# Optimization experiments

Measured on AMD Instinct MI355X. Metric: run time of the kernel, lower is better.

## Reference

```python
import jax, jax.numpy as jnp
import numpy as np

SIGMA = 25.0
HID, EMB = 64, 32
NBOX, BS = 10, 512
NPG = 3 * NBOX          # nodes per graph
N = BS * NPG            # total nodes


def _mlp2(h, W1, b1, W2, b2):
    return jax.nn.relu(h @ W1 + b1) @ W2 + b2


def _edge_conv(x, src, dst, W1, b1, W2, b2, n_nodes):
    # PyG EdgeConv: message = nn(cat([x_i, x_j - x_i])), aggr='max' at target i=dst
    xi = x[dst]
    xj = x[src]
    msg = _mlp2(jnp.concatenate([xi, xj - xi], axis=-1), W1, b1, W2, b2)
    return jax.ops.segment_max(msg, dst, num_segments=n_nodes)


def setup_inputs() -> dict:
    key = jax.random.key(0)
    k = jax.random.split(key, 16)
    w = lambda i, shape, s=0.1: jax.random.normal(k[i], shape, jnp.float32) * s
    # fully-connected directed edges (no self loops) within each of BS graphs
    ii, jj = np.meshgrid(np.arange(NPG), np.arange(NPG), indexing='ij')
    m = ii != jj
    off = (np.arange(BS) * NPG)[:, None]
    src = (ii[m][None, :] + off).reshape(-1)
    dst = (jj[m][None, :] + off).reshape(-1)
    edge_index = jnp.asarray(np.stack([src, dst]), dtype=jnp.int32)
    return {
        "x": jax.random.normal(k[0], (N, 2), jnp.float32),
        "t": jax.random.uniform(k[1], (BS, 1), jnp.float32, 1e-3, 1.0),
        "edge_index": edge_index,
        "n_box": NBOX,
        "gfp_W": jax.random.normal(k[2], (EMB // 2,), jnp.float32) * 30.0,
        "embed_W": w(3, (EMB, EMB)), "embed_b": jnp.zeros((EMB,), jnp.float32),
        "cat_emb": w(4, (3, EMB), 1.0), "cat_W": w(5, (EMB, EMB)), "cat_b": jnp.zeros((EMB,), jnp.float32),
        "init_W1": w(6, (2, HID)), "init_b1": jnp.zeros((HID,), jnp.float32),
        "init_W2": w(7, (HID, HID)), "init_b2": jnp.zeros((HID,), jnp.float32),
        "m1_W1": w(8, (2 * (HID + EMB), HID)), "m1_b1": jnp.zeros((HID,), jnp.float32),
        "m1_W2": w(9, (HID, HID)), "m1_b2": jnp.zeros((HID,), jnp.float32),
        "m2_W1": w(10, (2 * HID + 2 * EMB, HID)), "m2_b1": jnp.zeros((HID,), jnp.float32),
        "m2_W2": w(11, (HID, HID)), "m2_b2": jnp.zeros((HID,), jnp.float32),
        "m3_W1": w(12, (2 * HID + 2 * EMB, HID)), "m3_b1": jnp.zeros((HID,), jnp.float32),
        "m3_W2": w(13, (HID, 2)), "m3_b2": jnp.zeros((2,), jnp.float32),
    }


def reference(x, t, edge_index, n_box, gfp_W, embed_W, embed_b, cat_emb, cat_W, cat_b,
              init_W1, init_b1, init_W2, init_b2,
              m1_W1, m1_b1, m1_W2, m1_b2,
              m2_W1, m2_b1, m2_W2, m2_b2,
              m3_W1, m3_b1, m3_W2, m3_b2):
    n_nodes = x.shape[0]
    bs = t.shape[0]
    npg = 3 * n_box
    src, dst = edge_index[0], edge_index[1]
    # category embedding (mode='target'): pattern [0..0,1..1,2..2] tiled over graphs
    categories = jnp.tile(jnp.repeat(jnp.arange(3), n_box), bs)
    class_feat = jax.nn.relu(cat_emb[categories]) @ cat_W + cat_b          # [N, EMB]
    init_feat = jnp.concatenate(
        [_mlp2(x, init_W1, init_b1, init_W2, init_b2), class_feat], axis=-1)  # [N, HID+EMB]
    # Gaussian Fourier time embedding
    tp = t[:, 0]
    proj = tp[:, None] * gfp_W[None, :] * (2.0 * np.float32(np.pi))
    gfp = jnp.concatenate([jnp.sin(proj), jnp.cos(proj)], axis=-1)          # [bs, EMB]
    x_sigma = jax.nn.relu(jax.nn.relu(gfp) @ embed_W + embed_b)             # [bs, EMB]
    x_sigma = jnp.repeat(x_sigma, npg, axis=0)                              # [N, EMB]
    h = jax.nn.relu(_edge_conv(init_feat, src, dst, m1_W1, m1_b1, m1_W2, m1_b2, n_nodes))
    h = jnp.concatenate([h, x_sigma], axis=-1)
    h = jax.nn.relu(_edge_conv(h, src, dst, m2_W1, m2_b1, m2_W2, m2_b2, n_nodes))
    h = jnp.concatenate([h, x_sigma], axis=-1)
    h = _edge_conv(h, src, dst, m3_W1, m3_b1, m3_W2, m3_b2, n_nodes)        # [N, 2]
    # marginal_prob_std(t) = sqrt((sigma^{2t}-1)/(2 ln sigma)) per node
    t_node = jnp.repeat(tp, npg)[:, None]
    log_s = jnp.float32(np.log(SIGMA))
    std = jnp.sqrt((jnp.exp(2.0 * t_node * log_s) - 1.0) / (2.0 * log_s))
    return h / (std + 1e-7)
```

## Files before the change

kernel.cpp:

```cpp
#include <hip/hip_runtime.h>
#include <math.h>

constexpr int NPG  = 30;
constexpr int HID  = 64;
constexpr int EMB  = 32;
constexpr int FEAT = HID + EMB;
constexpr int BS   = 512;
constexpr int FROWH = 104;
constexpr int PROW  = 36;

constexpr int OFF_IW2  = 0;
constexpr int OFF_W1_1 = 4096;
constexpr int OFF_W1_2 = 16384;
constexpr int OFF_W1_3 = 28672;
constexpr int OFF_W2_1 = 40960;
constexpr int OFF_W2_2 = 45056;
constexpr int OFF_W2_3 = 49152;
constexpr int NHALF    = 51200;

typedef _Float16 half8 __attribute__((ext_vector_type(8)));
typedef __fp16   fp16x2 __attribute__((ext_vector_type(2)));
typedef float    f32x16 __attribute__((ext_vector_type(16)));

union HU  { unsigned u[4]; half8 h; };
union PK  { fp16x2 h2; unsigned u; };
union UPK { unsigned u; _Float16 h[2]; };

__device__ __forceinline__ void split8(const float* mv, half8& ah, half8& al) {
    #pragma unroll
    for (int d = 0; d < 4; d++) {
        auto ph = __builtin_amdgcn_cvt_pkrtz(mv[2*d], mv[2*d+1]);
        ah[2*d] = ph[0]; ah[2*d+1] = ph[1];
        float l0 = mv[2*d]   - (float)ph[0];
        float l1 = mv[2*d+1] - (float)ph[1];
        auto pl = __builtin_amdgcn_cvt_pkrtz(l0, l1);
        al[2*d] = pl[0]; al[2*d+1] = pl[1];
    }
}

__device__ __forceinline__ unsigned pkrne(float lo, float hi) {
    unsigned r;
    asm("v_fma_mixlo_f16 %0, %1, 1.0, 0" : "=v"(r) : "v"(lo));
    asm("v_fma_mixhi_f16 %0, %1, 1.0, 0" : "+v"(r) : "v"(hi));
    return r;
}

__device__ __forceinline__ unsigned pk_relu_add(unsigned a, unsigned b) {
    unsigned r;
    asm("v_pk_add_f16 %0, %1, %2" : "=v"(r) : "v"(a), "v"(b));
    asm("v_pk_max_f16 %0, %0, 0" : "+v"(r));
    return r;
}

__device__ __forceinline__ float dpp_xor1(float x) {
    return __int_as_float(__builtin_amdgcn_update_dpp(
        0, __float_as_int(x), 0xB1, 0xF, 0xF, true));
}

__global__ __launch_bounds__(256) void precompute_kernel(
    const float* __restrict__ t,
    const float* __restrict__ gfpW,
    const float* __restrict__ embW,
    const float* __restrict__ embb,
    const float* __restrict__ cat_emb,
    const float* __restrict__ catW,
    const float* __restrict__ catb,
    float* __restrict__ xs,
    float* __restrict__ cf3,
    float* __restrict__ stdv)
{
    int tid = blockIdx.x * blockDim.x + threadIdx.x;
    if (tid < BS) {
        float tp = t[tid];
        const float log_s = 3.2188758248682006f;
        stdv[tid] = sqrtf((expf(2.f * tp * log_s) - 1.f) / (2.f * log_s));

        float g[EMB];
        #pragma unroll
        for (int k = 0; k < EMB / 2; k++) {
            float pr = tp * gfpW[k] * 6.283185307179586f;
            g[k]           = sinf(pr);
            g[k + EMB / 2] = cosf(pr);
        }
        #pragma unroll
        for (int c = 0; c < EMB; c++) g[c] = fmaxf(g[c], 0.f);

        for (int o = 0; o < EMB; o++) {
            float acc = embb[o];
            #pragma unroll
            for (int c = 0; c < EMB; c++) acc = fmaf(g[c], embW[c * EMB + o], acc);
            xs[tid * EMB + o] = fmaxf(acc, 0.f);
        }
    } else if (tid < BS + 3 * EMB) {
        int idx = tid - BS;
        int r = idx >> 5, o = idx & 31;
        float acc = catb[o];
        #pragma unroll
        for (int c = 0; c < EMB; c++)
            acc = fmaf(fmaxf(cat_emb[r * EMB + c], 0.f), catW[c * EMB + o], acc);
        cf3[idx] = acc;
    }
}

__global__ __launch_bounds__(256) void convert_weights(
    const float* __restrict__ iW2,
    const float* __restrict__ W1_1, const float* __restrict__ W1_2,
    const float* __restrict__ W1_3,
    const float* __restrict__ W2_1, const float* __restrict__ W2_2,
    const float* __restrict__ W2_3,
    _Float16* __restrict__ outh)
{
    int idx = blockIdx.x * 256 + threadIdx.x;
    if (idx >= NHALF) return;
    float v;
    if (idx < OFF_W1_1) {
        int r = idx;
        int e = r & 7, cw = (r >> 3) & 31, hi = (r >> 8) & 1;
        int ks = (r >> 9) & 3, n = r >> 11;
        v = iW2[(16 * ks + 8 * hi + e) * HID + 32 * n + cw];
    } else if (idx < OFF_W2_1) {
        int r = idx - OFF_W1_1;
        int m = r / 12288; r %= 12288;
        const float* W1 = (m == 0) ? W1_1 : (m == 1) ? W1_2 : W1_3;
        int e = r & 7, cw = (r >> 3) & 31, hi = (r >> 8) & 1;
        int t2 = r >> 9;
        int ks = t2 % 6, np = t2 / 6;
        int rowoff = (np >= 2) ? FEAT : 0;
        int coloff = 32 * (np & 1);
        v = W1[(rowoff + 16 * ks + 8 * hi + e) * HID + coloff + cw];
    } else if (idx < OFF_W2_3) {
        int r = idx - OFF_W2_1;
        int m = r / 4096; r %= 4096;
        const float* W2 = (m == 0) ? W2_1 : W2_2;
        int e = r & 7, cw = (r >> 3) & 31, hi = (r >> 8) & 1;
        int ks = (r >> 9) & 3, n = r >> 11;
        v = W2[(16 * ks + 8 * hi + e) * HID + 32 * n + cw];
    } else {
        int r = idx - OFF_W2_3;
        int e = r & 7, cw = (r >> 3) & 31, hi = (r >> 8) & 1;
        int ks = (r >> 9) & 3;
        v = (cw < 2) ? W2_3[(16 * ks + 8 * hi + e) * 2 + cw] : 0.f;
    }
    outh[idx] = (_Float16)v;
}

__global__ __launch_bounds__(512, 4) void gnn_kernel(
    const float* __restrict__ xg,
    const float* __restrict__ iW1, const float* __restrict__ ib1,
    const float* __restrict__ ib2,
    const float* __restrict__ b1_1, const float* __restrict__ b2_1,
    const float* __restrict__ b1_2, const float* __restrict__ b2_2,
    const float* __restrict__ b1_3, const float* __restrict__ b2_3,
    const _Float16* __restrict__ hw,
    const float* __restrict__ xs_g,
    const float* __restrict__ cf3g,
    const float* __restrict__ stdv,
    float* __restrict__ out)
{
    const int g    = blockIdx.x;
    const int tid  = threadIdx.x;
    const int w    = tid >> 6;
    const int lane = tid & 63;
    const int cw   = lane & 31;
    const int hi   = lane >> 5;
    const int base = g * NPG;

    __shared__ __align__(16) unsigned slab[16 * 8 * 64];
    __shared__ __align__(16) _Float16 ftileh[32][FROWH];
    __shared__ __align__(16) unsigned ABp[32 * PROW];
    __shared__ __align__(16) unsigned Bp[32 * PROW];
    __shared__ float xs_s[EMB];

    float* slab32 = (float*)slab;

    if (tid < EMB) xs_s[tid] = xs_g[g * EMB + tid];

    if (w < 2) {
        int r = cw;
        float x0 = 0.f, x1 = 0.f;
        if (r < NPG) { x0 = xg[(base + r) * 2]; x1 = xg[(base + r) * 2 + 1]; }
        int n = w, coloff = 32 * n;
        f32x16 cc;
        #pragma unroll
        for (int z = 0; z < 16; z++) cc[z] = 0.f;
        #pragma unroll
        for (int ks = 0; ks < 4; ks++) {
            float mv[8];
            #pragma unroll
            for (int e = 0; e < 8; e++) {
                int k = 16 * ks + 8 * hi + e;
                mv[e] = fmaxf(fmaf(x1, iW1[HID + k], fmaf(x0, iW1[k], ib1[k])), 0.f);
            }
            half8 ah, al;
            split8(mv, ah, al);
            half8 wf = *(const half8*)&hw[OFF_IW2 + (((n * 4 + ks) * 2 + hi) * 32 + cw) * 8];
            cc = __builtin_amdgcn_mfma_f32_32x32x16_f16(ah, wf, cc, 0, 0, 0);
            cc = __builtin_amdgcn_mfma_f32_32x32x16_f16(al, wf, cc, 0, 0, 0);
        }
        float b2v = ib2[coloff + cw];
        #pragma unroll
        for (int rr = 0; rr < 16; rr++) {
            int row = (rr & 3) + 8 * (rr >> 2) + 4 * hi;
            if (row < NPG) ftileh[row][coloff + cw] = (_Float16)(cc[rr] + b2v);
        }
    }
    #pragma unroll
    for (int m = 0; m < 2; m++) {
        int idx = tid + 512 * m;
        if (idx < NPG * EMB) {
            int rr2 = idx >> 5, cc2 = idx & 31;
            ftileh[rr2][64 + cc2] = (_Float16)cf3g[(rr2 / 10) * EMB + cc2];
        }
    }
    __syncthreads();

    auto phase1AB = [&](const _Float16* __restrict__ W1f,
                        const float* __restrict__ b1) {
        if (w < 2) {
            const int n = __builtin_amdgcn_readfirstlane(w);
            f32x16 cA, cB;
            #pragma unroll
            for (int z = 0; z < 16; z++) { cA[z] = 0.f; cB[z] = 0.f; }
            #pragma unroll
            for (int ks = 0; ks < 6; ks++) {
                half8 af  = *(const half8*)&ftileh[cw][16 * ks + 8 * hi];
                half8 wfA = *(const half8*)&W1f[(((n * 6 + ks) * 2 + hi) * 32 + cw) * 8];
                half8 wfB = *(const half8*)&W1f[((((2 + n) * 6 + ks) * 2 + hi) * 32 + cw) * 8];
                cA = __builtin_amdgcn_mfma_f32_32x32x16_f16(af, wfA, cA, 0, 0, 0);
                cB = __builtin_amdgcn_mfma_f32_32x32x16_f16(af, wfB, cB, 0, 0, 0);
            }
            float b1v = b1[32 * n + cw];
            #pragma unroll
            for (int rr = 0; rr < 16; rr++) {
                float ab  = cA[rr] + b1v - cB[rr];
                float bb  = cB[rr];
                float abn = dpp_xor1(ab);
                float bbn = dpp_xor1(bb);
                int row = (rr & 3) + 8 * (rr >> 2) + 4 * hi;
                if ((cw & 1) == 0 && row < NPG) {
                    int idx = row * PROW + 16 * n + (cw >> 1);
                    ABp[idx] = pkrne(ab, abn);
                    Bp[idx]  = pkrne(bb, bbn);
                }
            }
        }
    };

    auto phase2_12 = [&](const half8 (&wf)[2][4], const float* __restrict__ b2) {
        const int s8 = __builtin_amdgcn_readfirstlane(w);
        float b2v[2] = { b2[cw], b2[32 + cw] };
        uint4 abp[4];
        #pragma unroll
        for (int ks = 0; ks < 4; ks++)
            abp[ks] = *(const uint4*)&ABp[cw * PROW + 8 * ks + 4 * hi];
        unsigned mxp[2][8];
        #pragma unroll
        for (int n = 0; n < 2; n++)
            #pragma unroll
            for (int d = 0; d < 8; d++) mxp[n][d] = 0xFC00FC00u;
        const bool selfh = (hi == ((s8 >> 2) & 1));

        #pragma unroll
        for (int m = 0; m < 4; m++) {
            int i = s8 + 8 * m;
            if (i < NPG) {
                const unsigned* bp = &Bp[i * PROW + 4 * hi];
                half8 am[4];
                #pragma unroll
                for (int ks = 0; ks < 4; ks++) {
                    uint4 bq = *(const uint4*)(bp + 8 * ks);
                    HU u;
                    u.u[0] = pk_relu_add(abp[ks].x, bq.x);
                    u.u[1] = pk_relu_add(abp[ks].y, bq.y);
                    u.u[2] = pk_relu_add(abp[ks].z, bq.z);
                    u.u[3] = pk_relu_add(abp[ks].w, bq.w);
                    am[ks] = u.h;
                }
                #pragma unroll
                for (int n = 0; n < 2; n++) {
                    f32x16 c;
                    #pragma unroll
                    for (int z = 0; z < 16; z++) c[z] = b2v[n];
                    #pragma unroll
                    for (int ks = 0; ks < 4; ks++)
                        c = __builtin_amdgcn_mfma_f32_32x32x16_f16(am[ks], wf[n][ks], c, 0, 0, 0);
                    switch (s8 & 3) {
                        case 0: c[4*m+0] = selfh ? -3.0e38f : c[4*m+0]; break;
                        case 1: c[4*m+1] = selfh ? -3.0e38f : c[4*m+1]; break;
                        case 2: c[4*m+2] = selfh ? -3.0e38f : c[4*m+2]; break;
                        default: c[4*m+3] = selfh ? -3.0e38f : c[4*m+3]; break;
                    }
                    #pragma unroll
                    for (int d = 0; d < 8; d++) {
                        PK pk; pk.h2 = __builtin_amdgcn_cvt_pkrtz(c[2*d], c[2*d+1]);
                        asm("v_pk_max_f16 %0, %0, %1" : "+v"(mxp[n][d]) : "v"(pk.u));
                    }
                }
            }
        }
        #pragma unroll
        for (int n = 0; n < 2; n++)
            #pragma unroll
            for (int d = 0; d < 8; d++)
                slab[(((n * 8 + d) * 8) + w) * 64 + lane] = mxp[n][d];
    };

    auto merge_12 = [&](bool installXS) {
        int rlane = tid & 63, rcw = rlane & 31, rhi = rlane >> 5;
        #pragma unroll
        for (int hh = 0; hh < 2; hh++) {
            int nd = (tid >> 6) + 8 * hh;
            unsigned mv = slab[(nd * 8 + 0) * 64 + rlane];
            #pragma unroll
            for (int ww = 1; ww < 8; ww++) {
                unsigned s = slab[(nd * 8 + ww) * 64 + rlane];
                asm("v_pk_max_f16 %0, %0, %1" : "+v"(mv) : "v"(s));
            }
            int n = nd >> 3, d = nd & 7;
            int col = 32 * n + rcw;
            UPK uu; uu.u = mv;
            int r0 = (2 * d & 3) + 8 * (d >> 1) + 4 * rhi;
            float v0 = fmaxf((float)uu.h[0], 0.f);
            float v1 = fmaxf((float)uu.h[1], 0.f);
            if (r0 < NPG)     ftileh[r0][col]     = (_Float16)v0;
            if (r0 + 1 < NPG) ftileh[r0 + 1][col] = (_Float16)v1;
        }
        if (installXS) {
            #pragma unroll
            for (int m = 0; m < 2; m++) {
                int idx = tid + 512 * m;
                if (idx < NPG * EMB) {
                    int rr2 = idx >> 5, cc2 = idx & 31;
                    ftileh[rr2][64 + cc2] = (_Float16)xs_s[cc2];
                }
            }
        }
    };

    {
        half8 wf[2][4];
        #pragma unroll
        for (int n = 0; n < 2; n++)
            #pragma unroll
            for (int ks = 0; ks < 4; ks++)
                wf[n][ks] = *(const half8*)&hw[OFF_W2_1 + (((n * 4 + ks) * 2 + hi) * 32 + cw) * 8];
        phase1AB(hw + OFF_W1_1, b1_1);
        __syncthreads();
        phase2_12(wf, b2_1);
        __syncthreads();
        merge_12(true);
        __syncthreads();
    }
    {
        half8 wf[2][4];
        #pragma unroll
        for (int n = 0; n < 2; n++)
            #pragma unroll
            for (int ks = 0; ks < 4; ks++)
                wf[n][ks] = *(const half8*)&hw[OFF_W2_2 + (((n * 4 + ks) * 2 + hi) * 32 + cw) * 8];
        phase1AB(hw + OFF_W1_2, b1_2);
        __syncthreads();
        phase2_12(wf, b2_2);
        __syncthreads();
        merge_12(false);
        __syncthreads();
    }
    {
        half8 wf3[4];
        #pragma unroll
        for (int ks = 0; ks < 4; ks++)
            wf3[ks] = *(const half8*)&hw[OFF_W2_3 + ((ks * 2 + hi) * 32 + cw) * 8];
        phase1AB(hw + OFF_W1_3, b1_3);
        __syncthreads();

        const int s8 = __builtin_amdgcn_readfirstlane(w);
        uint4 abp[4];
        #pragma unroll
        for (int ks = 0; ks < 4; ks++)
            abp[ks] = *(const uint4*)&ABp[cw * PROW + 8 * ks + 4 * hi];
        f32x16 mx;
        #pragma unroll
        for (int z = 0; z < 16; z++) mx[z] = -3.0e38f;
        const bool selfh = (hi == ((s8 >> 2) & 1));

        #pragma unroll
        for (int m = 0; m < 4; m++) {
            int i = s8 + 8 * m;
            if (i < NPG) {
                const unsigned* bp = &Bp[i * PROW + 4 * hi];
                f32x16 c;
                #pragma unroll
                for (int z = 0; z < 16; z++) c[z] = 0.f;
                #pragma unroll
                for (int ks = 0; ks < 4; ks++) {
                    uint4 bq = *(const uint4*)(bp + 8 * ks);
                    HU u;
                    u.u[0] = pk_relu_add(abp[ks].x, bq.x);
                    u.u[1] = pk_relu_add(abp[ks].y, bq.y);
                    u.u[2] = pk_relu_add(abp[ks].z, bq.z);
                    u.u[3] = pk_relu_add(abp[ks].w, bq.w);
                    c = __builtin_amdgcn_mfma_f32_32x32x16_f16(u.h, wf3[ks], c, 0, 0, 0);
                }
                switch (s8 & 3) {
                    case 0: c[4*m+0] = selfh ? -3.0e38f : c[4*m+0]; break;
                    case 1: c[4*m+1] = selfh ? -3.0e38f : c[4*m+1]; break;
                    case 2: c[4*m+2] = selfh ? -3.0e38f : c[4*m+2]; break;
                    default: c[4*m+3] = selfh ? -3.0e38f : c[4*m+3]; break;
                }
                #pragma unroll
                for (int rr = 0; rr < 16; rr++) mx[rr] = fmaxf(mx[rr], c[rr]);
            }
        }
        #pragma unroll
        for (int rr = 0; rr < 16; rr++)
            slab32[(rr * 8 + w) * 64 + lane] = mx[rr];
    }
    __syncthreads();
    {
        int rlane = tid & 63, rcw = rlane & 31, rhi = rlane >> 5;
        float inv = 1.f / (stdv[g] + 1e-7f);
        #pragma unroll
        for (int hh = 0; hh < 2; hh++) {
            int rr = (tid >> 6) + 8 * hh;
            float mv = slab32[(rr * 8 + 0) * 64 + rlane];
            #pragma unroll
            for (int ww = 1; ww < 8; ww++)
                mv = fmaxf(mv, slab32[(rr * 8 + ww) * 64 + rlane]);
            if (rcw < 2) {
                int row = (rr & 3) + 8 * (rr >> 2) + 4 * rhi;
                if (row < NPG)
                    out[(base + row) * 2 + rcw] = (mv + b2_3[rcw]) * inv;
            }
        }
    }
}

extern "C" void kernel_launch(void* const* d_in, const int* in_sizes, int n_in,
                              void* d_out, int out_size, void* d_ws, size_t ws_size,
                              hipStream_t stream)
{
    const float* x       = (const float*)d_in[0];
    const float* t       = (const float*)d_in[1];
    const float* gfpW    = (const float*)d_in[4];
    const float* embW    = (const float*)d_in[5];
    const float* embb    = (const float*)d_in[6];
    const float* cat_emb = (const float*)d_in[7];
    const float* catW    = (const float*)d_in[8];
    const float* catb    = (const float*)d_in[9];
    const float* iW1     = (const float*)d_in[10];
    const float* ib1     = (const float*)d_in[11];
    const float* iW2     = (const float*)d_in[12];
    const float* ib2     = (const float*)d_in[13];
    const float* W1_1    = (const float*)d_in[14];
    const float* b1_1    = (const float*)d_in[15];
    const float* W2_1    = (const float*)d_in[16];
    const float* b2_1    = (const float*)d_in[17];
    const float* W1_2    = (const float*)d_in[18];
    const float* b1_2    = (const float*)d_in[19];
    const float* W2_2    = (const float*)d_in[20];
    const float* b2_2    = (const float*)d_in[21];
    const float* W1_3    = (const float*)d_in[22];
    const float* b1_3    = (const float*)d_in[23];
    const float* W2_3    = (const float*)d_in[24];
    const float* b2_3    = (const float*)d_in[25];

    const int bs = in_sizes[1];

    float* ws   = (float*)d_ws;
    float* xs   = ws;
    float* cf3  = ws + BS * EMB;
    float* stdv = ws + BS * EMB + 3 * EMB;
    _Float16* hw = (_Float16*)(ws + 17024);

    precompute_kernel<<<3, 256, 0, stream>>>(t, gfpW, embW, embb, cat_emb, catW,
                                             catb, xs, cf3, stdv);
    convert_weights<<<(NHALF + 255) / 256, 256, 0, stream>>>(
        iW2, W1_1, W1_2, W1_3, W2_1, W2_2, W2_3, hw);
    gnn_kernel<<<bs, 512, 0, stream>>>(x, iW1, ib1, ib2,
                                       b1_1, b2_1, b1_2, b2_2, b1_3, b2_3,
                                       hw, xs, cf3, stdv, (float*)d_out);
}
```

Baseline: 39.12 us.

## Fuse time/category embedding precompute into GNN kernel and tree-reduce max merges

Removes the separate precompute kernel launch and computes the Gaussian Fourier time embedding, std inverse and category features inside each GNN block, using otherwise idle waves 2 and 3 during the initial MLP phase. This eliminates one launch and a global round-trip for xs/cf3/stdv. Each block now redundantly computes the category features and its own time embedding. The per-node max merges across waves are also rewritten as a load-all-then-tree reduction to shorten dependency chains.

```diff
diff --git a/kernel.cpp b/kernel.cpp
--- a/kernel.cpp
+++ b/kernel.cpp
@@ -5,7 +5,6 @@
 constexpr int HID  = 64;
 constexpr int EMB  = 32;
 constexpr int FEAT = HID + EMB;
-constexpr int BS   = 512;
 constexpr int FROWH = 104;
 constexpr int PROW  = 36;
 
@@ -52,54 +51,15 @@
     return r;
 }
 
+__device__ __forceinline__ unsigned pk_max2(unsigned a, unsigned b) {
+    unsigned r;
+    asm("v_pk_max_f16 %0, %1, %2" : "=v"(r) : "v"(a), "v"(b));
+    return r;
+}
+
 __device__ __forceinline__ float dpp_xor1(float x) {
     return __int_as_float(__builtin_amdgcn_update_dpp(
         0, __float_as_int(x), 0xB1, 0xF, 0xF, true));
-}
-
-__global__ __launch_bounds__(256) void precompute_kernel(
-    const float* __restrict__ t,
-    const float* __restrict__ gfpW,
-    const float* __restrict__ embW,
-    const float* __restrict__ embb,
-    const float* __restrict__ cat_emb,
-    const float* __restrict__ catW,
-    const float* __restrict__ catb,
-    float* __restrict__ xs,
-    float* __restrict__ cf3,
-    float* __restrict__ stdv)
-{
-    int tid = blockIdx.x * blockDim.x + threadIdx.x;
-    if (tid < BS) {
-        float tp = t[tid];
-        const float log_s = 3.2188758248682006f;
-        stdv[tid] = sqrtf((expf(2.f * tp * log_s) - 1.f) / (2.f * log_s));
-
-        float g[EMB];
-        #pragma unroll
-        for (int k = 0; k < EMB / 2; k++) {
-            float pr = tp * gfpW[k] * 6.283185307179586f;
-            g[k]           = sinf(pr);
-            g[k + EMB / 2] = cosf(pr);
-        }
-        #pragma unroll
-        for (int c = 0; c < EMB; c++) g[c] = fmaxf(g[c], 0.f);
-
-        for (int o = 0; o < EMB; o++) {
-            float acc = embb[o];
-            #pragma unroll
-            for (int c = 0; c < EMB; c++) acc = fmaf(g[c], embW[c * EMB + o], acc);
-            xs[tid * EMB + o] = fmaxf(acc, 0.f);
-        }
-    } else if (tid < BS + 3 * EMB) {
-        int idx = tid - BS;
-        int r = idx >> 5, o = idx & 31;
-        float acc = catb[o];
-        #pragma unroll
-        for (int c = 0; c < EMB; c++)
-            acc = fmaf(fmaxf(cat_emb[r * EMB + c], 0.f), catW[c * EMB + o], acc);
-        cf3[idx] = acc;
-    }
 }
 
 __global__ __launch_bounds__(256) void convert_weights(
@@ -146,15 +106,19 @@
 
 __global__ __launch_bounds__(512, 4) void gnn_kernel(
     const float* __restrict__ xg,
+    const float* __restrict__ tg,
+    const float* __restrict__ gfpW,
+    const float* __restrict__ embW,
+    const float* __restrict__ embb,
+    const float* __restrict__ cat_emb,
+    const float* __restrict__ catW,
+    const float* __restrict__ catb,
     const float* __restrict__ iW1, const float* __restrict__ ib1,
     const float* __restrict__ ib2,
     const float* __restrict__ b1_1, const float* __restrict__ b2_1,
     const float* __restrict__ b1_2, const float* __restrict__ b2_2,
     const float* __restrict__ b1_3, const float* __restrict__ b2_3,
     const _Float16* __restrict__ hw,
-    const float* __restrict__ xs_g,
-    const float* __restrict__ cf3g,
-    const float* __restrict__ stdv,
     float* __restrict__ out)
 {
     const int g    = blockIdx.x;
@@ -170,10 +134,9 @@
     __shared__ __align__(16) unsigned ABp[32 * PROW];
     __shared__ __align__(16) unsigned Bp[32 * PROW];
     __shared__ float xs_s[EMB];
+    __shared__ float inv_s;
 
     float* slab32 = (float*)slab;
-
-    if (tid < EMB) xs_s[tid] = xs_g[g * EMB + tid];
 
     if (w < 2) {
         int r = cw;
@@ -203,13 +166,39 @@
             int row = (rr & 3) + 8 * (rr >> 2) + 4 * hi;
             if (row < NPG) ftileh[row][coloff + cw] = (_Float16)(cc[rr] + b2v);
         }
-    }
-    #pragma unroll
-    for (int m = 0; m < 2; m++) {
-        int idx = tid + 512 * m;
-        if (idx < NPG * EMB) {
-            int rr2 = idx >> 5, cc2 = idx & 31;
-            ftileh[rr2][64 + cc2] = (_Float16)cf3g[(rr2 / 10) * EMB + cc2];
+    } else if (w == 2) {
+        float tp = tg[g];
+        if (lane < EMB) {
+            int o = lane;
+            float acc = embb[o];
+            #pragma unroll 4
+            for (int c = 0; c < EMB; c++) {
+                float pr = tp * gfpW[c & 15] * 6.283185307179586f;
+                float gc = (c < 16) ? sinf(pr) : cosf(pr);
+                gc = fmaxf(gc, 0.f);
+                acc = fmaf(gc, embW[c * EMB + o], acc);
+            }
+            xs_s[o] = fmaxf(acc, 0.f);
+        } else if (lane == 32) {
+            const float log_s = 3.2188758248682006f;
+            float std = sqrtf((expf(2.f * tp * log_s) - 1.f) / (2.f * log_s));
+            inv_s = 1.f / (std + 1e-7f);
+        }
+    } else if (w == 3) {
+        #pragma unroll
+        for (int m = 0; m < 2; m++) {
+            int idx = (m == 0) ? lane : 64 + lane;
+            if (idx < 3 * EMB) {
+                int r = idx >> 5, o = idx & 31;
+                float acc = catb[o];
+                #pragma unroll 8
+                for (int c = 0; c < EMB; c++)
+                    acc = fmaf(fmaxf(cat_emb[r * EMB + c], 0.f), catW[c * EMB + o], acc);
+                _Float16 hv = (_Float16)acc;
+                #pragma unroll
+                for (int j = 0; j < 10; j++)
+                    ftileh[r * 10 + j][64 + o] = hv;
+            }
         }
     }
     __syncthreads();
@@ -307,15 +296,20 @@
 
     auto merge_12 = [&](bool installXS) {
         int rlane = tid & 63, rcw = rlane & 31, rhi = rlane >> 5;
+        unsigned v[2][8];
         #pragma unroll
         for (int hh = 0; hh < 2; hh++) {
             int nd = (tid >> 6) + 8 * hh;
-            unsigned mv = slab[(nd * 8 + 0) * 64 + rlane];
-            #pragma unroll
-            for (int ww = 1; ww < 8; ww++) {
-                unsigned s = slab[(nd * 8 + ww) * 64 + rlane];
-                asm("v_pk_max_f16 %0, %0, %1" : "+v"(mv) : "v"(s));
-            }
+            #pragma unroll
+            for (int ww = 0; ww < 8; ww++)
+                v[hh][ww] = slab[(nd * 8 + ww) * 64 + rlane];
+        }
+        #pragma unroll
+        for (int hh = 0; hh < 2; hh++) {
+            int nd = (tid >> 6) + 8 * hh;
+            unsigned mv = pk_max2(
+                pk_max2(pk_max2(v[hh][0], v[hh][1]), pk_max2(v[hh][2], v[hh][3])),
+                pk_max2(pk_max2(v[hh][4], v[hh][5]), pk_max2(v[hh][6], v[hh][7])));
             int n = nd >> 3, d = nd & 7;
             int col = 32 * n + rcw;
             UPK uu; uu.u = mv;
@@ -418,14 +412,19 @@
     __syncthreads();
     {
         int rlane = tid & 63, rcw = rlane & 31, rhi = rlane >> 5;
-        float inv = 1.f / (stdv[g] + 1e-7f);
+        float inv = inv_s;
         #pragma unroll
         for (int hh = 0; hh < 2; hh++) {
             int rr = (tid >> 6) + 8 * hh;
-            float mv = slab32[(rr * 8 + 0) * 64 + rlane];
-            #pragma unroll
-            for (int ww = 1; ww < 8; ww++)
-                mv = fmaxf(mv, slab32[(rr * 8 + ww) * 64 + rlane]);
+            float m0 = fmaxf(slab32[(rr * 8 + 0) * 64 + rlane],
+                             slab32[(rr * 8 + 1) * 64 + rlane]);
+            float m1 = fmaxf(slab32[(rr * 8 + 2) * 64 + rlane],
+                             slab32[(rr * 8 + 3) * 64 + rlane]);
+            float m2 = fmaxf(slab32[(rr * 8 + 4) * 64 + rlane],
+                             slab32[(rr * 8 + 5) * 64 + rlane]);
+            float m3 = fmaxf(slab32[(rr * 8 + 6) * 64 + rlane],
+                             slab32[(rr * 8 + 7) * 64 + rlane]);
+            float mv = fmaxf(fmaxf(m0, m1), fmaxf(m2, m3));
             if (rcw < 2) {
                 int row = (rr & 3) + 8 * (rr >> 2) + 4 * rhi;
                 if (row < NPG)
@@ -466,17 +465,12 @@
 
     const int bs = in_sizes[1];
 
-    float* ws   = (float*)d_ws;
-    float* xs   = ws;
-    float* cf3  = ws + BS * EMB;
-    float* stdv = ws + BS * EMB + 3 * EMB;
-    _Float16* hw = (_Float16*)(ws + 17024);
-
-    precompute_kernel<<<3, 256, 0, stream>>>(t, gfpW, embW, embb, cat_emb, catW,
-                                             catb, xs, cf3, stdv);
+    _Float16* hw = (_Float16*)d_ws;
+
     convert_weights<<<(NHALF + 255) / 256, 256, 0, stream>>>(
         iW2, W1_1, W1_2, W1_3, W2_1, W2_2, W2_3, hw);
-    gnn_kernel<<<bs, 512, 0, stream>>>(x, iW1, ib1, ib2,
+    gnn_kernel<<<bs, 512, 0, stream>>>(x, t, gfpW, embW, embb, cat_emb, catW, catb,
+                                       iW1, ib1, ib2,
                                        b1_1, b2_1, b1_2, b2_2, b1_3, b2_3,
-                                       hw, xs, cf3, stdv, (float*)d_out);
-}
+                                       hw, (float*)d_out);
+}
```

Result: faster. 35.92 us (-8.2%).
